# Kernel tuning notes

Measured on AMD Instinct MI355X. Metric: run time of the kernel, lower is better.

Reference implementation:

```python
import jax, jax.numpy as jnp
import numpy as np

EPS_BN = 1e-5
NEG = -9e15


def _bn_train(x, g, b):
    # x: [B, C, N]; training-mode BatchNorm1d with batch stats (biased var)
    m = jnp.mean(x, axis=(0, 2), keepdims=True)
    v = jnp.mean((x - m) ** 2, axis=(0, 2), keepdims=True)
    return (x - m) * jax.lax.rsqrt(v + EPS_BN) * g[None, :, None] + b[None, :, None]


def _conv1x1(w, x, b=None):
    # w: [O, C], x: [B, C, N] -> [B, O, N]
    y = jnp.einsum('oc,bcn->bon', w, x)
    if b is not None:
        y = y + b[None, :, None]
    return y


def _sa_layer(x, maskb, qk_w, v_w, v_b, t_w, t_b, bn_g, bn_b):
    # x: [B, C, N], maskb: [B, N] bool
    q = jnp.einsum('hc,bcn->bhn', qk_w, x)          # shared q/k weights
    energy = jnp.einsum('bhn,bhm->bnm', q, q)        # [B, N, N]
    pair = maskb[:, :, None] & maskb[:, None, :]
    energy = jnp.where(pair, energy, NEG)
    attn = jax.nn.softmax(energy, axis=-1)
    attn = attn / (1e-9 + jnp.sum(attn, axis=1, keepdims=True))  # L1 renorm over dim=1
    x_v = _conv1x1(v_w, x, v_b)                      # [B, C, N]
    x_r = jnp.einsum('bcn,bnm->bcm', x_v, attn)      # bmm(x_v, attention)
    t = _conv1x1(t_w, x - x_r, t_b)
    x_r = jax.nn.relu(_bn_train(t, bn_g, bn_b))
    return x + x_r


def setup_inputs() -> dict:
    key = jax.random.key(0)
    ks = jax.random.split(key, 16)
    B, C, N = 16, 256, 2048
    H = C // 4
    s = 0.05
    inp = {
        'x': jax.random.normal(ks[0], (B, C, N), jnp.float32),
        'mask': jax.random.randint(ks[1], (B, N), 0, 2, jnp.int32),
        'conv1_w': jax.random.normal(ks[2], (C, C), jnp.float32) * s,
        'conv2_w': jax.random.normal(ks[3], (C, C), jnp.float32) * s,
        'bn1_g': jnp.ones((C,), jnp.float32),
        'bn1_b': jnp.zeros((C,), jnp.float32),
        'bn2_g': jnp.ones((C,), jnp.float32),
        'bn2_b': jnp.zeros((C,), jnp.float32),
        'sa_qk_w': jax.random.normal(ks[4], (4, H, C), jnp.float32) * s,
        'sa_v_w': jax.random.normal(ks[5], (4, C, C), jnp.float32) * s,
        'sa_v_b': jax.random.normal(ks[6], (4, C), jnp.float32) * s,
        'sa_t_w': jax.random.normal(ks[7], (4, C, C), jnp.float32) * s,
        'sa_t_b': jax.random.normal(ks[8], (4, C), jnp.float32) * s,
        'sa_bn_g': jnp.ones((4, C), jnp.float32),
        'sa_bn_b': jnp.zeros((4, C), jnp.float32),
    }
    return inp


def reference(x, mask, conv1_w, conv2_w, bn1_g, bn1_b, bn2_g, bn2_b,
              sa_qk_w, sa_v_w, sa_v_b, sa_t_w, sa_t_b, sa_bn_g, sa_bn_b):
    maskb = mask.astype(bool)
    x = jax.nn.relu(_bn_train(_conv1x1(conv1_w, x), bn1_g, bn1_b))
    x = jax.nn.relu(_bn_train(_conv1x1(conv2_w, x), bn2_g, bn2_b))
    outs = []
    for i in range(4):
        x = _sa_layer(x, maskb, sa_qk_w[i], sa_v_w[i], sa_v_b[i],
                      sa_t_w[i], sa_t_b[i], sa_bn_g[i], sa_bn_b[i])
        outs.append(x)
    return jnp.concatenate(outs, axis=1)  # [B, 4C, N]
```

## Files before the change

kernel.cpp:

```cpp
#include <hip/hip_runtime.h>
#include <math.h>

#define BB 16
#define CC 256
#define NN 2048
#define HH 64
#define NEGV (-9.0e15f)
#define ATTSC 4096.0f
#define ATTINV (1.0f/4096.0f)

typedef _Float16 f16x8 __attribute__((ext_vector_type(8)));
typedef float f32x4 __attribute__((ext_vector_type(4)));

__device__ __forceinline__ f32x4 mfma16(f16x8 a, f16x8 b, f32x4 c) {
  return __builtin_amdgcn_mfma_f32_16x16x32_f16(a, b, c, 0, 0, 0);
}
__device__ __forceinline__ unsigned short f2h(float f) {
  _Float16 h = (_Float16)f;
  return __builtin_bit_cast(unsigned short, h);
}
__device__ __forceinline__ float h2f(unsigned short u) {
  return (float)__builtin_bit_cast(_Float16, u);
}
__device__ __forceinline__ unsigned short* sp(unsigned short* base, int row, int colh) {
  return (unsigned short*)((char*)base + (row << 7) + (((colh << 1)) ^ ((row & 7) << 4)));
}
__device__ __forceinline__ const unsigned short* spc(const unsigned short* base, int row, int colh) {
  return (const unsigned short*)((const char*)base + (row << 7) + (((colh << 1)) ^ ((row & 7) << 4)));
}

__global__ __launch_bounds__(256)
void castw_kernel(const float* __restrict__ in, unsigned short* __restrict__ out, int n)
{
  const int i = blockIdx.x*256 + threadIdx.x;
  if (i < n) out[i] = f2h(in[i]);
}

__global__ __launch_bounds__(256)
void tcast_kernel(const float* __restrict__ src, long sstride,
                  unsigned short* __restrict__ dst)
{
  const int b = blockIdx.z, n0 = blockIdx.x*64, c0 = blockIdx.y*64;
  const int t = threadIdx.x;
  __shared__ float tile[64][66];
  const float* sb = src + (long)b*sstride;
  #pragma unroll
  for (int p = 0; p < 4; p++) {
    const int cr = (t>>4) + p*16;
    const int nq = (t&15)*4;
    const float4 v = *(const float4*)&sb[(long)(c0+cr)*NN + n0 + nq];
    tile[cr][nq+0] = v.x; tile[cr][nq+1] = v.y;
    tile[cr][nq+2] = v.z; tile[cr][nq+3] = v.w;
  }
  __syncthreads();
  unsigned short* db = dst + (long)b*NN*CC;
  #pragma unroll
  for (int p = 0; p < 4; p++) {
    const int nr = (t>>4) + p*16;
    const int cq = (t&15)*4;
    ushort4 o;
    o.x = f2h(tile[cq+0][nr]); o.y = f2h(tile[cq+1][nr]);
    o.z = f2h(tile[cq+2][nr]); o.w = f2h(tile[cq+3][nr]);
    *(ushort4*)&db[(long)(n0+nr)*CC + c0 + cq] = o;
  }
}

__global__ __launch_bounds__(256)
void gemm_xw_kernel(const unsigned short* __restrict__ A,
                    const unsigned short* __restrict__ W,
                    const float* __restrict__ bias,
                    unsigned short* __restrict__ out, int ocols)
{
  const int n0 = blockIdx.x*64, o0 = blockIdx.y*64, b = blockIdx.z;
  const int t = threadIdx.x;
  const int w = t >> 6, l = t & 63, lr = l & 15, lg = l >> 4;
  const int wr = w >> 1, wc = w & 1;
  __shared__ unsigned short Al[64][72];
  __shared__ unsigned short Bl[64][72];
  const unsigned short* Ab = A + ((long)b*NN + n0)*CC;
  const int srow = t >> 3, sg = t & 7;
  f32x4 acc[2][2];
  #pragma unroll
  for (int i = 0; i < 2; i++)
    #pragma unroll
    for (int j = 0; j < 2; j++) acc[i][j] = f32x4{0.f,0.f,0.f,0.f};

  for (int kt = 0; kt < 4; kt++) {
    const int k0 = kt*64;
    const uint4 a0 = *(const uint4*)&Ab[(long)srow*CC + k0 + sg*8];
    const uint4 a1 = *(const uint4*)&Ab[(long)(srow+32)*CC + k0 + sg*8];
    const uint4 w0 = *(const uint4*)&W[(long)(o0+srow)*CC + k0 + sg*8];
    const uint4 w1 = *(const uint4*)&W[(long)(o0+srow+32)*CC + k0 + sg*8];
    __syncthreads();
    *(uint4*)&Al[srow][sg*8] = a0;  *(uint4*)&Al[srow+32][sg*8] = a1;
    *(uint4*)&Bl[srow][sg*8] = w0;  *(uint4*)&Bl[srow+32][sg*8] = w1;
    __syncthreads();
    #pragma unroll
    for (int kf = 0; kf < 2; kf++) {
      f16x8 af0 = *(const f16x8*)&Al[wr*32 + lr]     [kf*32 + lg*8];
      f16x8 af1 = *(const f16x8*)&Al[wr*32 + 16 + lr][kf*32 + lg*8];
      f16x8 bf0 = *(const f16x8*)&Bl[wc*32 + lr]     [kf*32 + lg*8];
      f16x8 bf1 = *(const f16x8*)&Bl[wc*32 + 16 + lr][kf*32 + lg*8];
      acc[0][0] = mfma16(af0, bf0, acc[0][0]);
      acc[0][1] = mfma16(af0, bf1, acc[0][1]);
      acc[1][0] = mfma16(af1, bf0, acc[1][0]);
      acc[1][1] = mfma16(af1, bf1, acc[1][1]);
    }
  }
  #pragma unroll
  for (int j = 0; j < 2; j++) {
    const int oc = o0 + wc*32 + j*16 + lr;
    const float bo = bias ? bias[oc] : 0.f;
    #pragma unroll
    for (int i = 0; i < 2; i++) {
      const int nb = n0 + wr*32 + i*16 + lg*4;
      #pragma unroll
      for (int r = 0; r < 4; r++)
        out[((long)b*NN + nb + r)*ocols + oc] = f2h(acc[i][j][r] + bo);
    }
  }
}

__global__ __launch_bounds__(256)
void gemm_wx_kernel(const unsigned short* __restrict__ W,
                    const unsigned short* __restrict__ X,
                    const float* __restrict__ bias,
                    unsigned short* __restrict__ out)
{
  const int n0 = blockIdx.x*64, o0 = blockIdx.y*64, b = blockIdx.z;
  const int t = threadIdx.x;
  const int w = t >> 6, l = t & 63, lr = l & 15, lg = l >> 4;
  const int wr = w >> 1, wc = w & 1;
  __shared__ unsigned short Al[64][72];
  __shared__ unsigned short Bl[64][72];
  const unsigned short* Xb = X + ((long)b*NN + n0)*CC;
  const int srow = t >> 3, sg = t & 7;
  f32x4 acc[2][2];
  #pragma unroll
  for (int i = 0; i < 2; i++)
    #pragma unroll
    for (int j = 0; j < 2; j++) acc[i][j] = f32x4{0.f,0.f,0.f,0.f};

  for (int kt = 0; kt < 4; kt++) {
    const int k0 = kt*64;
    const uint4 w0 = *(const uint4*)&W[(long)(o0+srow)*CC + k0 + sg*8];
    const uint4 w1 = *(const uint4*)&W[(long)(o0+srow+32)*CC + k0 + sg*8];
    const uint4 x0 = *(const uint4*)&Xb[(long)srow*CC + k0 + sg*8];
    const uint4 x1 = *(const uint4*)&Xb[(long)(srow+32)*CC + k0 + sg*8];
    __syncthreads();
    *(uint4*)&Al[srow][sg*8] = w0;  *(uint4*)&Al[srow+32][sg*8] = w1;
    *(uint4*)&Bl[srow][sg*8] = x0;  *(uint4*)&Bl[srow+32][sg*8] = x1;
    __syncthreads();
    #pragma unroll
    for (int kf = 0; kf < 2; kf++) {
      f16x8 af0 = *(const f16x8*)&Al[wr*32 + lr]     [kf*32 + lg*8];
      f16x8 af1 = *(const f16x8*)&Al[wr*32 + 16 + lr][kf*32 + lg*8];
      f16x8 bf0 = *(const f16x8*)&Bl[wc*32 + lr]     [kf*32 + lg*8];
      f16x8 bf1 = *(const f16x8*)&Bl[wc*32 + 16 + lr][kf*32 + lg*8];
      acc[0][0] = mfma16(af0, bf0, acc[0][0]);
      acc[0][1] = mfma16(af0, bf1, acc[0][1]);
      acc[1][0] = mfma16(af1, bf0, acc[1][0]);
      acc[1][1] = mfma16(af1, bf1, acc[1][1]);
    }
  }
  #pragma unroll
  for (int j = 0; j < 2; j++) {
    const int nc = n0 + wc*32 + j*16 + lr;
    #pragma unroll
    for (int i = 0; i < 2; i++) {
      #pragma unroll
      for (int r = 0; r < 4; r++) {
        const int oc = o0 + wr*32 + i*16 + lg*4 + r;
        out[((long)b*CC + oc)*NN + nc] = f2h(acc[i][j][r] + bias[oc]);
      }
    }
  }
}

__global__ __launch_bounds__(256)
void rowstat_kernel(const unsigned short* __restrict__ qT, const int* __restrict__ mask,
                    float* __restrict__ rmax, float* __restrict__ rinv)
{
  const int bid = blockIdx.x;
  const int swz = (bid & 7)*64 + (bid >> 3);
  const int b  = swz >> 5;
  const int n0 = (swz & 31) * 64;
  const int t = threadIdx.x, w = t>>6, l = t&63, lr = l&15, lg = l>>4;
  __shared__ unsigned short qs[64*64];
  __shared__ int ml[64];
  const int srow = t>>3, sg = t&7;
  const unsigned short* qbase = qT + (long)b*NN*HH;
  *(uint4*)sp(qs, srow,    sg*8) = *(const uint4*)&qbase[(long)(n0+srow)*HH + sg*8];
  *(uint4*)sp(qs, srow+32, sg*8) = *(const uint4*)&qbase[(long)(n0+srow+32)*HH + sg*8];
  int maskn[4];
  #pragma unroll
  for (int r = 0; r < 4; r++) maskn[r] = mask[(long)b*NN + n0 + w*16 + lg*4 + r];
  __syncthreads();
  f16x8 af0 = *(const f16x8*)spc(qs, w*16 + lr, lg*8);
  f16x8 af1 = *(const f16x8*)spc(qs, w*16 + lr, 32 + lg*8);
  float mx[4], sm[4];
  #pragma unroll
  for (int r = 0; r < 4; r++) { mx[r] = -INFINITY; sm[r] = 0.f; }

  for (int m0 = 0; m0 < NN; m0 += 64) {
    __syncthreads();
    *(uint4*)sp(qs, srow,    sg*8) = *(const uint4*)&qbase[(long)(m0+srow)*HH + sg*8];
    *(uint4*)sp(qs, srow+32, sg*8) = *(const uint4*)&qbase[(long)(m0+srow+32)*HH + sg*8];
    if (t < 64) ml[t] = mask[(long)b*NN + m0 + t];
    __syncthreads();
    float sv[4][4];
    #pragma unroll
    for (int tm = 0; tm < 4; tm++) {
      f32x4 s = f32x4{0.f,0.f,0.f,0.f};
      s = mfma16(af0, *(const f16x8*)spc(qs, tm*16 + lr, lg*8),      s);
      s = mfma16(af1, *(const f16x8*)spc(qs, tm*16 + lr, 32 + lg*8), s);
      const int cm = ml[tm*16 + lr];
      #pragma unroll
      for (int r = 0; r < 4; r++) sv[tm][r] = (maskn[r] && cm) ? s[r] : NEGV;
    }
    #pragma unroll
    for (int r = 0; r < 4; r++) {
      const float tmx = fmaxf(fmaxf(sv[0][r], sv[1][r]), fmaxf(sv[2][r], sv[3][r]));
      const float nm  = fmaxf(mx[r], tmx);
      sm[r] = sm[r]*__expf(mx[r]-nm)
            + __expf(sv[0][r]-nm) + __expf(sv[1][r]-nm)
            + __expf(sv[2][r]-nm) + __expf(sv[3][r]-nm);
      mx[r] = nm;
    }
  }
  #pragma unroll
  for (int off = 1; off < 16; off <<= 1) {
    #pragma unroll
    for (int r = 0; r < 4; r++) {
      const float om = __shfl_xor(mx[r], off, 64);
      const float os = __shfl_xor(sm[r], off, 64);
      const float nm = fmaxf(mx[r], om);
      sm[r] = sm[r]*__expf(mx[r]-nm) + os*__expf(om-nm);
      mx[r] = nm;
    }
  }
  if (lr == 0) {
    #pragma unroll
    for (int r = 0; r < 4; r++) {
      const long idx = (long)b*NN + n0 + w*16 + lg*4 + r;
      rmax[idx] = mx[r];
      rinv[idx] = 1.f/sm[r];
    }
  }
}

__global__ __launch_bounds__(256)
void yatt_kernel(const unsigned short* __restrict__ qT, const unsigned short* __restrict__ xv,
                 const int* __restrict__ mask, const float* __restrict__ rmax,
                 const float* __restrict__ rinv, unsigned short* __restrict__ xrTh,
                 float* __restrict__ csum)
{
  const int bid = blockIdx.x;
  const int swz = (bid & 7)*64 + (bid >> 3);
  const int b  = swz >> 5;
  const int m0 = (swz & 31) * 64;
  const int t = threadIdx.x, w = t>>6, l = t&63, lr = l&15, lg = l>>4;
  __shared__ unsigned short qn[64*64];
  __shared__ unsigned short at[64*64];
  __shared__ float rml[64], ril[64];
  __shared__ int mrl[64];
  const int srow = t>>3, sg = t&7;
  const unsigned short* qbase = qT + (long)b*NN*HH;
  const unsigned short* xvb = xv + (long)b*CC*NN;

  *(uint4*)sp(at, srow,    sg*8) = *(const uint4*)&qbase[(long)(m0+srow)*HH + sg*8];
  *(uint4*)sp(at, srow+32, sg*8) = *(const uint4*)&qbase[(long)(m0+srow+32)*HH + sg*8];
  int maskm[4];
  #pragma unroll
  for (int r = 0; r < 4; r++) maskm[r] = mask[(long)b*NN + m0 + w*16 + lg*4 + r];
  __syncthreads();
  f16x8 am0 = *(const f16x8*)spc(at, w*16 + lr, lg*8);
  f16x8 am1 = *(const f16x8*)spc(at, w*16 + lr, 32 + lg*8);

  f32x4 acc[4][4];
  #pragma unroll
  for (int mi = 0; mi < 4; mi++)
    #pragma unroll
    for (int ci = 0; ci < 4; ci++) acc[mi][ci] = f32x4{0.f,0.f,0.f,0.f};
  float cs[4] = {0.f, 0.f, 0.f, 0.f};

  for (int nc = 0; nc < NN; nc += 64) {
    __syncthreads();
    *(uint4*)sp(qn, srow,    sg*8) = *(const uint4*)&qbase[(long)(nc+srow)*HH + sg*8];
    *(uint4*)sp(qn, srow+32, sg*8) = *(const uint4*)&qbase[(long)(nc+srow+32)*HH + sg*8];
    if (t < 64) {
      rml[t] = rmax[(long)b*NN + nc + t];
      ril[t] = rinv[(long)b*NN + nc + t];
      mrl[t] = mask[(long)b*NN + nc + t];
    }
    f16x8 xb0[4], xb1[4];
    #pragma unroll
    for (int ci = 0; ci < 4; ci++) {
      const unsigned short* xp = &xvb[(long)(w*64 + ci*16 + lr)*NN + nc];
      xb0[ci] = *(const f16x8*)(xp + lg*8);
      xb1[ci] = *(const f16x8*)(xp + 32 + lg*8);
    }
    __syncthreads();
    #pragma unroll
    for (int tn = 0; tn < 4; tn++) {
      f32x4 s = f32x4{0.f,0.f,0.f,0.f};
      s = mfma16(am0, *(const f16x8*)spc(qn, tn*16 + lr, lg*8),      s);
      s = mfma16(am1, *(const f16x8*)spc(qn, tn*16 + lr, 32 + lg*8), s);
      const int nn = tn*16 + lr;
      const int cm = mrl[nn];
      const float rm = rml[nn], ri = ril[nn];
      #pragma unroll
      for (int r = 0; r < 4; r++) {
        const float vm = (maskm[r] && cm) ? s[r] : NEGV;
        const float a_ = __expf(vm - rm) * ri;
        cs[r] += a_;
        *sp(at, w*16 + lg*4 + r, nn) = f2h(a_ * ATTSC);
      }
    }
    __syncthreads();
    {
      f16x8 aa[4];
      #pragma unroll
      for (int mi = 0; mi < 4; mi++) aa[mi] = *(const f16x8*)spc(at, mi*16 + lr, lg*8);
      #pragma unroll
      for (int ci = 0; ci < 4; ci++)
        #pragma unroll
        for (int mi = 0; mi < 4; mi++)
          acc[mi][ci] = mfma16(aa[mi], xb0[ci], acc[mi][ci]);
      #pragma unroll
      for (int mi = 0; mi < 4; mi++) aa[mi] = *(const f16x8*)spc(at, mi*16 + lr, 32 + lg*8);
      #pragma unroll
      for (int ci = 0; ci < 4; ci++)
        #pragma unroll
        for (int mi = 0; mi < 4; mi++)
          acc[mi][ci] = mfma16(aa[mi], xb1[ci], acc[mi][ci]);
    }
  }
  #pragma unroll
  for (int mi = 0; mi < 4; mi++)
    #pragma unroll
    for (int ci = 0; ci < 4; ci++)
      #pragma unroll
      for (int r = 0; r < 4; r++)
        xrTh[((long)b*NN + m0 + mi*16 + lg*4 + r)*CC + w*64 + ci*16 + lr] =
            f2h(acc[mi][ci][r] * ATTINV);
  #pragma unroll
  for (int off = 1; off < 16; off <<= 1) {
    #pragma unroll
    for (int r = 0; r < 4; r++) cs[r] += __shfl_xor(cs[r], off, 64);
  }
  if (lr == 0) {
    #pragma unroll
    for (int r = 0; r < 4; r++)
      csum[(long)b*NN + m0 + w*16 + lg*4 + r] = cs[r];
  }
}

__global__ __launch_bounds__(256)
void diff_kernel(const unsigned short* __restrict__ xT, const unsigned short* __restrict__ xrTh,
                 const float* __restrict__ csumv, unsigned short* __restrict__ dT)
{
  const long i = (long)blockIdx.x*256 + threadIdx.x;
  const long base = i*8;
  const long row = base >> 8;
  const float inv = 1.f/(1e-9f + csumv[row]);
  const uint4 xu = *(const uint4*)&xT[base];
  const uint4 yu = *(const uint4*)&xrTh[base];
  const unsigned short* xs = (const unsigned short*)&xu;
  const unsigned short* ys = (const unsigned short*)&yu;
  uint4 ou;
  unsigned short* os = (unsigned short*)&ou;
  #pragma unroll
  for (int j = 0; j < 8; j++) os[j] = f2h(h2f(xs[j]) - h2f(ys[j])*inv);
  *(uint4*)&dT[base] = ou;
}

__global__ __launch_bounds__(256)
void bnstatsA_kernel(const unsigned short* __restrict__ tTh, float* __restrict__ part)
{
  const int k = blockIdx.x;
  const int c = threadIdx.x;
  float s = 0.f, sq = 0.f;
  const long r0 = (long)k*128;
  for (int r = 0; r < 128; r++) {
    const float v = h2f(tTh[(r0 + r)*CC + c]);
    s += v; sq += v*v;
  }
  part[(long)k*CC + c] = s;
  part[(long)(256 + k)*CC + c] = sq;
}

__global__ __launch_bounds__(1024)
void bnstatsB_kernel(const float* __restrict__ part,
                     float* __restrict__ mean, float* __restrict__ istd)
{
  const int t = threadIdx.x, c = t & 255, q = t >> 8;
  float s = 0.f, sq = 0.f;
  for (int k = q*64; k < q*64 + 64; k++) {
    s  += part[(long)k*CC + c];
    sq += part[(long)(256 + k)*CC + c];
  }
  __shared__ float ls[4][256], lq[4][256];
  ls[q][c] = s; lq[q][c] = sq;
  __syncthreads();
  if (q == 0) {
    s  = ls[0][c] + ls[1][c] + ls[2][c] + ls[3][c];
    sq = lq[0][c] + lq[1][c] + lq[2][c] + lq[3][c];
    const float mu = s / (float)(BB*NN);
    mean[c] = mu;
    istd[c] = rsqrtf(sq/(float)(BB*NN) - mu*mu + 1e-5f);
  }
}

__global__ __launch_bounds__(256)
void bnapplyA_kernel(const unsigned short* __restrict__ tTh, const float* __restrict__ mean,
                     const float* __restrict__ istd, const float* __restrict__ g,
                     const float* __restrict__ bt, unsigned short* __restrict__ xTo)
{
  __shared__ float sc[CC], sh[CC];
  const int t = threadIdx.x;
  {
    const float is = istd[t], gg = g[t];
    sc[t] = is*gg; sh[t] = bt[t] - mean[t]*is*gg;
  }
  __syncthreads();
  const long i = (long)blockIdx.x*256 + t;
  const long base = i*8;
  const int c8 = (int)(base & 255);
  const uint4 v = *(const uint4*)&tTh[base];
  const unsigned short* hs = (const unsigned short*)&v;
  uint4 ou;
  unsigned short* os = (unsigned short*)&ou;
  #pragma unroll
  for (int j = 0; j < 8; j++)
    os[j] = f2h(fmaxf(h2f(hs[j])*sc[c8+j] + sh[c8+j], 0.f));
  *(uint4*)&xTo[base] = ou;
}

__global__ __launch_bounds__(256)
void bnfuse_kernel(const unsigned short* __restrict__ tTh, const float* __restrict__ mean,
                   const float* __restrict__ istd, const float* __restrict__ g,
                   const float* __restrict__ bt, const float* __restrict__ resid,
                   long rstride, float* __restrict__ outp, long ostride,
                   unsigned short* __restrict__ xtn)
{
  const int b = blockIdx.z, n0 = blockIdx.x*64, c0 = blockIdx.y*64;
  const int t = threadIdx.x;
  __shared__ float tile[64][66];
  const unsigned short* tb_ = tTh + ((long)b*NN + n0)*CC;
  const int cq = (t&15)*4;
  float scv[4], shv[4];
  #pragma unroll
  for (int j = 0; j < 4; j++) {
    const int c = c0 + cq + j;
    const float is = istd[c], gg = g[c];
    scv[j] = is*gg; shv[j] = bt[c] - mean[c]*is*gg;
  }
  #pragma unroll
  for (int p = 0; p < 4; p++) {
    const int nr = (t>>4) + p*16;
    const ushort4 v = *(const ushort4*)&tb_[(long)nr*CC + c0 + cq];
    tile[cq+0][nr] = fmaxf(h2f(v.x)*scv[0] + shv[0], 0.f);
    tile[cq+1][nr] = fmaxf(h2f(v.y)*scv[1] + shv[1], 0.f);
    tile[cq+2][nr] = fmaxf(h2f(v.z)*scv[2] + shv[2], 0.f);
    tile[cq+3][nr] = fmaxf(h2f(v.w)*scv[3] + shv[3], 0.f);
  }
  __syncthreads();
  const int nq = (t&15)*4;
  #pragma unroll
  for (int p = 0; p < 4; p++) {
    const int cr = (t>>4) + p*16;
    float4 o;
    o.x = tile[cr][nq+0]; o.y = tile[cr][nq+1];
    o.z = tile[cr][nq+2]; o.w = tile[cr][nq+3];
    if (resid) {
      const float4 rv = *(const float4*)&resid[(long)b*rstride + (long)(c0+cr)*NN + n0 + nq];
      o.x += rv.x; o.y += rv.y; o.z += rv.z; o.w += rv.w;
    }
    *(float4*)&outp[(long)b*ostride + (long)(c0+cr)*NN + n0 + nq] = o;
    tile[cr][nq+0] = o.x; tile[cr][nq+1] = o.y;
    tile[cr][nq+2] = o.z; tile[cr][nq+3] = o.w;
  }
  if (xtn) {
    __syncthreads();
    #pragma unroll
    for (int p = 0; p < 4; p++) {
      const int nr = (t>>4) + p*16;
      ushort4 o;
      o.x = f2h(tile[cq+0][nr]); o.y = f2h(tile[cq+1][nr]);
      o.z = f2h(tile[cq+2][nr]); o.w = f2h(tile[cq+3][nr]);
      *(ushort4*)&xtn[((long)b*NN + n0+nr)*CC + c0 + cq] = o;
    }
  }
}

extern "C" void kernel_launch(void* const* d_in, const int* in_sizes, int n_in,
                              void* d_out, int out_size, void* d_ws, size_t ws_size,
                              hipStream_t stream)
{
  const float* x_in   = (const float*)d_in[0];
  const int*   mask   = (const int*)d_in[1];
  const float* conv1w = (const float*)d_in[2];
  const float* conv2w = (const float*)d_in[3];
  const float* bn1g   = (const float*)d_in[4];
  const float* bn1b   = (const float*)d_in[5];
  const float* bn2g   = (const float*)d_in[6];
  const float* bn2b   = (const float*)d_in[7];
  const float* qkw    = (const float*)d_in[8];
  const float* vw     = (const float*)d_in[9];
  const float* vb     = (const float*)d_in[10];
  const float* tw     = (const float*)d_in[11];
  const float* tb     = (const float*)d_in[12];
  const float* bng    = (const float*)d_in[13];
  const float* bnb    = (const float*)d_in[14];
  float* out = (float*)d_out;

  const long BCN = (long)BB*CC*NN;
  const long CN  = (long)CC*NN;
  char* p = (char*)d_ws;
  unsigned short* xTa  = (unsigned short*)p; p += BCN*2;
  unsigned short* xTb  = (unsigned short*)p; p += BCN*2;
  unsigned short* qTb  = (unsigned short*)p; p += (long)BB*NN*HH*2;
  unsigned short* xvb  = (unsigned short*)p; p += BCN*2;
  unsigned short* tTh  = (unsigned short*)p; p += BCN*2;
  unsigned short* xrTh = (unsigned short*)p; p += BCN*2;
  float* xbuf  = (float*)p; p += BCN*4;
  float* rmaxb = (float*)p; p += (long)BB*NN*4;
  float* rinvb = (float*)p; p += (long)BB*NN*4;
  float* csumb = (float*)p; p += (long)BB*NN*4;
  float* partb = (float*)p; p += 512L*CC*4;
  float* meanb = (float*)p; p += CC*4;
  float* istdb = (float*)p; p += CC*4;
  unsigned short* wc1 = (unsigned short*)p; p += (long)CC*CC*2;
  unsigned short* wc2 = (unsigned short*)p; p += (long)CC*CC*2;
  unsigned short* wqk = (unsigned short*)p; p += 4L*HH*CC*2;
  unsigned short* wv  = (unsigned short*)p; p += 4L*CC*CC*2;
  unsigned short* wt  = (unsigned short*)p; p += 4L*CC*CC*2;

  const dim3 gT(NN/64, CC/64, BB);
  const dim3 gQ(NN/64, 1, BB);
  const dim3 gAtt(512);
  const dim3 blk(256);

  castw_kernel<<<dim3(256), blk, 0, stream>>>(conv1w, wc1, CC*CC);
  castw_kernel<<<dim3(256), blk, 0, stream>>>(conv2w, wc2, CC*CC);
  castw_kernel<<<dim3(256), blk, 0, stream>>>(qkw, wqk, 4*HH*CC);
  castw_kernel<<<dim3(1024), blk, 0, stream>>>(vw, wv, 4*CC*CC);
  castw_kernel<<<dim3(1024), blk, 0, stream>>>(tw, wt, 4*CC*CC);

  tcast_kernel<<<gT, blk, 0, stream>>>(x_in, CN, xTa);
  gemm_xw_kernel<<<gT, blk, 0, stream>>>(xTa, wc1, nullptr, tTh, CC);
  bnstatsA_kernel<<<dim3(256), blk, 0, stream>>>(tTh, partb);
  bnstatsB_kernel<<<dim3(1), dim3(1024), 0, stream>>>(partb, meanb, istdb);
  bnapplyA_kernel<<<dim3(4096), blk, 0, stream>>>(tTh, meanb, istdb, bn1g, bn1b, xTb);
  gemm_xw_kernel<<<gT, blk, 0, stream>>>(xTb, wc2, nullptr, tTh, CC);
  bnstatsA_kernel<<<dim3(256), blk, 0, stream>>>(tTh, partb);
  bnstatsB_kernel<<<dim3(1), dim3(1024), 0, stream>>>(partb, meanb, istdb);
  bnfuse_kernel<<<gT, blk, 0, stream>>>(tTh, meanb, istdb, bn2g, bn2b,
                                        nullptr, 0, xbuf, CN, xTa);

  unsigned short* cur = xTa;
  unsigned short* nxt = xTb;
  for (int i = 0; i < 4; i++) {
    gemm_xw_kernel<<<gQ, blk, 0, stream>>>(cur, wqk + (long)i*HH*CC, nullptr, qTb, HH);
    rowstat_kernel<<<gAtt, blk, 0, stream>>>(qTb, mask, rmaxb, rinvb);
    gemm_wx_kernel<<<gT, blk, 0, stream>>>(wv + (long)i*CC*CC, cur, vb + (long)i*CC, xvb);
    yatt_kernel<<<gAtt, blk, 0, stream>>>(qTb, xvb, mask, rmaxb, rinvb, xrTh, csumb);
    diff_kernel<<<dim3(4096), blk, 0, stream>>>(cur, xrTh, csumb, xvb);
    gemm_xw_kernel<<<gT, blk, 0, stream>>>(xvb, wt + (long)i*CC*CC, tb + (long)i*CC, tTh, CC);
    bnstatsA_kernel<<<dim3(256), blk, 0, stream>>>(tTh, partb);
    bnstatsB_kernel<<<dim3(1), dim3(1024), 0, stream>>>(partb, meanb, istdb);
    const float* resid = (i == 0) ? xbuf : (out + (long)(i-1)*CN);
    const long rstr = (i == 0) ? CN : 4*CN;
    bnfuse_kernel<<<gT, blk, 0, stream>>>(tTh, meanb, istdb,
                                          bng + (long)i*CC, bnb + (long)i*CC,
                                          resid, rstr, out + (long)i*CN, 4*CN,
                                          (i < 3) ? nxt : nullptr);
    unsigned short* tmp = cur; cur = nxt; nxt = tmp;
  }

  (void)in_sizes; (void)n_in; (void)out_size; (void)ws_size;
}
```

Measured before the change: 773.3 us.

## Split attention rowstat and yatt across more blocks, fuse diff into T-conv GEMM

The rowstat kernel now splits the key dimension into four partial passes (2048 blocks). It reads q straight from global memory instead of LDS, and a new rowcomb kernel merges the partial max/sum pairs. The yatt kernel splits the channel dimension into two halves (1024 blocks) and computes keys from register-resident m-side q. Its column-sum reduction now goes through LDS. The separate diff kernel is removed by folding the x - xr/csum subtraction into a new gemm_dxw GEMM's operand load, in exchange for recomputing QK^T twice in yatt and an extra launch.

New measurement: 1.131 ms. 1.46x slower.

```diff
diff --git a/kernel.cpp b/kernel.cpp
--- a/kernel.cpp
+++ b/kernel.cpp
@@ -122,6 +122,82 @@
 }
 
 __global__ __launch_bounds__(256)
+void gemm_dxw_kernel(const unsigned short* __restrict__ X,
+                     const unsigned short* __restrict__ XR,
+                     const float* __restrict__ csumv,
+                     const unsigned short* __restrict__ W,
+                     const float* __restrict__ bias,
+                     unsigned short* __restrict__ out)
+{
+  const int n0 = blockIdx.x*64, o0 = blockIdx.y*64, b = blockIdx.z;
+  const int t = threadIdx.x;
+  const int w = t >> 6, l = t & 63, lr = l & 15, lg = l >> 4;
+  const int wr = w >> 1, wc = w & 1;
+  __shared__ unsigned short Al[64][72];
+  __shared__ unsigned short Bl[64][72];
+  const unsigned short* Xb  = X  + ((long)b*NN + n0)*CC;
+  const unsigned short* XRb = XR + ((long)b*NN + n0)*CC;
+  const int srow = t >> 3, sg = t & 7;
+  const float inv0 = 1.f/(1e-9f + csumv[(long)b*NN + n0 + srow]);
+  const float inv1 = 1.f/(1e-9f + csumv[(long)b*NN + n0 + srow + 32]);
+  f32x4 acc[2][2];
+  #pragma unroll
+  for (int i = 0; i < 2; i++)
+    #pragma unroll
+    for (int j = 0; j < 2; j++) acc[i][j] = f32x4{0.f,0.f,0.f,0.f};
+
+  for (int kt = 0; kt < 4; kt++) {
+    const int k0 = kt*64;
+    const uint4 xa  = *(const uint4*)&Xb [(long)srow*CC + k0 + sg*8];
+    const uint4 xra = *(const uint4*)&XRb[(long)srow*CC + k0 + sg*8];
+    const uint4 xb_ = *(const uint4*)&Xb [(long)(srow+32)*CC + k0 + sg*8];
+    const uint4 xrb = *(const uint4*)&XRb[(long)(srow+32)*CC + k0 + sg*8];
+    const uint4 w0 = *(const uint4*)&W[(long)(o0+srow)*CC + k0 + sg*8];
+    const uint4 w1 = *(const uint4*)&W[(long)(o0+srow+32)*CC + k0 + sg*8];
+    uint4 da, db_;
+    {
+      const unsigned short* xs = (const unsigned short*)&xa;
+      const unsigned short* rs = (const unsigned short*)&xra;
+      unsigned short* ds = (unsigned short*)&da;
+      #pragma unroll
+      for (int j = 0; j < 8; j++) ds[j] = f2h(h2f(xs[j]) - h2f(rs[j])*inv0);
+      xs = (const unsigned short*)&xb_;
+      rs = (const unsigned short*)&xrb;
+      ds = (unsigned short*)&db_;
+      #pragma unroll
+      for (int j = 0; j < 8; j++) ds[j] = f2h(h2f(xs[j]) - h2f(rs[j])*inv1);
+    }
+    __syncthreads();
+    *(uint4*)&Al[srow][sg*8] = da;  *(uint4*)&Al[srow+32][sg*8] = db_;
+    *(uint4*)&Bl[srow][sg*8] = w0;  *(uint4*)&Bl[srow+32][sg*8] = w1;
+    __syncthreads();
+    #pragma unroll
+    for (int kf = 0; kf < 2; kf++) {
+      f16x8 af0 = *(const f16x8*)&Al[wr*32 + lr]     [kf*32 + lg*8];
+      f16x8 af1 = *(const f16x8*)&Al[wr*32 + 16 + lr][kf*32 + lg*8];
+      f16x8 bf0 = *(const f16x8*)&Bl[wc*32 + lr]     [kf*32 + lg*8];
+      f16x8 bf1 = *(const f16x8*)&Bl[wc*32 + 16 + lr][kf*32 + lg*8];
+      acc[0][0] = mfma16(af0, bf0, acc[0][0]);
+      acc[0][1] = mfma16(af0, bf1, acc[0][1]);
+      acc[1][0] = mfma16(af1, bf0, acc[1][0]);
+      acc[1][1] = mfma16(af1, bf1, acc[1][1]);
+    }
+  }
+  #pragma unroll
+  for (int j = 0; j < 2; j++) {
+    const int oc = o0 + wc*32 + j*16 + lr;
+    const float bo = bias[oc];
+    #pragma unroll
+    for (int i = 0; i < 2; i++) {
+      const int nb = n0 + wr*32 + i*16 + lg*4;
+      #pragma unroll
+      for (int r = 0; r < 4; r++)
+        out[((long)b*NN + nb + r)*CC + oc] = f2h(acc[i][j][r] + bo);
+    }
+  }
+}
+
+__global__ __launch_bounds__(256)
 void gemm_wx_kernel(const unsigned short* __restrict__ W,
                     const unsigned short* __restrict__ X,
                     const float* __restrict__ bias,
@@ -179,44 +255,39 @@
 
 __global__ __launch_bounds__(256)
 void rowstat_kernel(const unsigned short* __restrict__ qT, const int* __restrict__ mask,
-                    float* __restrict__ rmax, float* __restrict__ rinv)
+                    float* __restrict__ pmax, float* __restrict__ psum)
 {
   const int bid = blockIdx.x;
-  const int swz = (bid & 7)*64 + (bid >> 3);
-  const int b  = swz >> 5;
-  const int n0 = (swz & 31) * 64;
+  const int sbid = (bid & 7)*256 + (bid >> 3);
+  const int b = sbid >> 7;
+  const int r_ = sbid & 127;
+  const int split = r_ >> 5;
+  const int nt4 = r_ & 31;
   const int t = threadIdx.x, w = t>>6, l = t&63, lr = l&15, lg = l>>4;
-  __shared__ unsigned short qs[64*64];
-  __shared__ int ml[64];
-  const int srow = t>>3, sg = t&7;
+  const int n0w = nt4*64 + w*16;
   const unsigned short* qbase = qT + (long)b*NN*HH;
-  *(uint4*)sp(qs, srow,    sg*8) = *(const uint4*)&qbase[(long)(n0+srow)*HH + sg*8];
-  *(uint4*)sp(qs, srow+32, sg*8) = *(const uint4*)&qbase[(long)(n0+srow+32)*HH + sg*8];
-  int maskn[4];
-  #pragma unroll
-  for (int r = 0; r < 4; r++) maskn[r] = mask[(long)b*NN + n0 + w*16 + lg*4 + r];
-  __syncthreads();
-  f16x8 af0 = *(const f16x8*)spc(qs, w*16 + lr, lg*8);
-  f16x8 af1 = *(const f16x8*)spc(qs, w*16 + lr, 32 + lg*8);
+  const unsigned short* qnp = &qbase[(long)(n0w + lr)*HH];
+  const f16x8 a0 = *(const f16x8*)(qnp + lg*8);
+  const f16x8 a1 = *(const f16x8*)(qnp + 32 + lg*8);
+  const int4 mn4 = *(const int4*)&mask[(long)b*NN + n0w + lg*4];
+  const int mn[4] = {mn4.x, mn4.y, mn4.z, mn4.w};
   float mx[4], sm[4];
   #pragma unroll
   for (int r = 0; r < 4; r++) { mx[r] = -INFINITY; sm[r] = 0.f; }
 
-  for (int m0 = 0; m0 < NN; m0 += 64) {
-    __syncthreads();
-    *(uint4*)sp(qs, srow,    sg*8) = *(const uint4*)&qbase[(long)(m0+srow)*HH + sg*8];
-    *(uint4*)sp(qs, srow+32, sg*8) = *(const uint4*)&qbase[(long)(m0+srow+32)*HH + sg*8];
-    if (t < 64) ml[t] = mask[(long)b*NN + m0 + t];
-    __syncthreads();
+  for (int c = 0; c < 8; c++) {
+    const int m0 = split*512 + c*64;
     float sv[4][4];
     #pragma unroll
     for (int tm = 0; tm < 4; tm++) {
-      f32x4 s = f32x4{0.f,0.f,0.f,0.f};
-      s = mfma16(af0, *(const f16x8*)spc(qs, tm*16 + lr, lg*8),      s);
-      s = mfma16(af1, *(const f16x8*)spc(qs, tm*16 + lr, 32 + lg*8), s);
-      const int cm = ml[tm*16 + lr];
-      #pragma unroll
-      for (int r = 0; r < 4; r++) sv[tm][r] = (maskn[r] && cm) ? s[r] : NEGV;
+      const unsigned short* qmp = &qbase[(long)(m0 + tm*16 + lr)*HH];
+      f16x8 b0 = *(const f16x8*)(qmp + lg*8);
+      f16x8 b1 = *(const f16x8*)(qmp + 32 + lg*8);
+      f32x4 s = mfma16(a0, b0, f32x4{0.f,0.f,0.f,0.f});
+      s = mfma16(a1, b1, s);
+      const int cm = mask[(long)b*NN + m0 + tm*16 + lr];
+      #pragma unroll
+      for (int r = 0; r < 4; r++) sv[tm][r] = (mn[r] && cm) ? s[r] : NEGV;
     }
     #pragma unroll
     for (int r = 0; r < 4; r++) {
@@ -242,11 +313,27 @@
   if (lr == 0) {
     #pragma unroll
     for (int r = 0; r < 4; r++) {
-      const long idx = (long)b*NN + n0 + w*16 + lg*4 + r;
-      rmax[idx] = mx[r];
-      rinv[idx] = 1.f/sm[r];
-    }
-  }
+      const long idx = (long)split*BB*NN + (long)b*NN + n0w + lg*4 + r;
+      pmax[idx] = mx[r];
+      psum[idx] = sm[r];
+    }
+  }
+}
+
+__global__ __launch_bounds__(256)
+void rowcomb_kernel(const float* __restrict__ pmax, const float* __restrict__ psum,
+                    float* __restrict__ rmaxo, float* __restrict__ rinvo)
+{
+  const long i = (long)blockIdx.x*256 + threadIdx.x;
+  const long BN = (long)BB*NN;
+  float m = pmax[i];
+  #pragma unroll
+  for (int k = 1; k < 4; k++) m = fmaxf(m, pmax[(long)k*BN + i]);
+  float s = 0.f;
+  #pragma unroll
+  for (int k = 0; k < 4; k++) s += psum[(long)k*BN + i]*__expf(pmax[(long)k*BN + i] - m);
+  rmaxo[i] = m;
+  rinvo[i] = 1.f/s;
 }
 
 __global__ __launch_bounds__(256)
@@ -256,123 +343,109 @@
                  float* __restrict__ csum)
 {
   const int bid = blockIdx.x;
-  const int swz = (bid & 7)*64 + (bid >> 3);
-  const int b  = swz >> 5;
-  const int m0 = (swz & 31) * 64;
+  const int swz = (bid & 7)*128 + (bid >> 3);
+  const int b  = swz >> 6;
+  const int r_ = swz & 63;
+  const int m0 = (r_ >> 1) * 64;
+  const int ch = r_ & 1;
   const int t = threadIdx.x, w = t>>6, l = t&63, lr = l&15, lg = l>>4;
-  __shared__ unsigned short qn[64*64];
+
   __shared__ unsigned short at[64*64];
-  __shared__ float rml[64], ril[64];
-  __shared__ int mrl[64];
-  const int srow = t>>3, sg = t&7;
+  __shared__ float csred[4][4][16];
+
   const unsigned short* qbase = qT + (long)b*NN*HH;
   const unsigned short* xvb = xv + (long)b*CC*NN;
 
-  *(uint4*)sp(at, srow,    sg*8) = *(const uint4*)&qbase[(long)(m0+srow)*HH + sg*8];
-  *(uint4*)sp(at, srow+32, sg*8) = *(const uint4*)&qbase[(long)(m0+srow+32)*HH + sg*8];
-  int maskm[4];
-  #pragma unroll
-  for (int r = 0; r < 4; r++) maskm[r] = mask[(long)b*NN + m0 + w*16 + lg*4 + r];
-  __syncthreads();
-  f16x8 am0 = *(const f16x8*)spc(at, w*16 + lr, lg*8);
-  f16x8 am1 = *(const f16x8*)spc(at, w*16 + lr, 32 + lg*8);
-
-  f32x4 acc[4][4];
+  f16x8 bq0[4], bq1[4];
+  int mcolv[4];
+  #pragma unroll
+  for (int tm = 0; tm < 4; tm++) {
+    const unsigned short* qp = &qbase[(long)(m0 + tm*16 + lr)*HH];
+    bq0[tm] = *(const f16x8*)(qp + lg*8);
+    bq1[tm] = *(const f16x8*)(qp + 32 + lg*8);
+    mcolv[tm] = mask[(long)b*NN + m0 + tm*16 + lr];
+  }
+
+  f32x4 acc[4][2];
   #pragma unroll
   for (int mi = 0; mi < 4; mi++)
     #pragma unroll
-    for (int ci = 0; ci < 4; ci++) acc[mi][ci] = f32x4{0.f,0.f,0.f,0.f};
+    for (int ci = 0; ci < 2; ci++) acc[mi][ci] = f32x4{0.f,0.f,0.f,0.f};
   float cs[4] = {0.f, 0.f, 0.f, 0.f};
+  const int nb = w*16 + lg*4;
 
   for (int nc = 0; nc < NN; nc += 64) {
-    __syncthreads();
-    *(uint4*)sp(qn, srow,    sg*8) = *(const uint4*)&qbase[(long)(nc+srow)*HH + sg*8];
-    *(uint4*)sp(qn, srow+32, sg*8) = *(const uint4*)&qbase[(long)(nc+srow+32)*HH + sg*8];
-    if (t < 64) {
-      rml[t] = rmax[(long)b*NN + nc + t];
-      ril[t] = rinv[(long)b*NN + nc + t];
-      mrl[t] = mask[(long)b*NN + nc + t];
-    }
-    f16x8 xb0[4], xb1[4];
-    #pragma unroll
-    for (int ci = 0; ci < 4; ci++) {
-      const unsigned short* xp = &xvb[(long)(w*64 + ci*16 + lr)*NN + nc];
+    const unsigned short* qnp = &qbase[(long)(nc + w*16 + lr)*HH];
+    const f16x8 a0 = *(const f16x8*)(qnp + lg*8);
+    const f16x8 a1 = *(const f16x8*)(qnp + 32 + lg*8);
+    f16x8 xb0[2], xb1[2];
+    #pragma unroll
+    for (int ci = 0; ci < 2; ci++) {
+      const unsigned short* xp = &xvb[(long)(ch*128 + w*32 + ci*16 + lr)*NN + nc];
       xb0[ci] = *(const f16x8*)(xp + lg*8);
       xb1[ci] = *(const f16x8*)(xp + 32 + lg*8);
     }
-    __syncthreads();
-    #pragma unroll
-    for (int tn = 0; tn < 4; tn++) {
-      f32x4 s = f32x4{0.f,0.f,0.f,0.f};
-      s = mfma16(am0, *(const f16x8*)spc(qn, tn*16 + lr, lg*8),      s);
-      s = mfma16(am1, *(const f16x8*)spc(qn, tn*16 + lr, 32 + lg*8), s);
-      const int nn = tn*16 + lr;
-      const int cm = mrl[nn];
-      const float rm = rml[nn], ri = ril[nn];
+    const float4 rm4 = *(const float4*)&rmax[(long)b*NN + nc + nb];
+    const float4 ri4 = *(const float4*)&rinv[(long)b*NN + nc + nb];
+    const int4   mn4 = *(const int4*)&mask[(long)b*NN + nc + nb];
+    const float rmv[4] = {rm4.x, rm4.y, rm4.z, rm4.w};
+    const float riv[4] = {ri4.x, ri4.y, ri4.z, ri4.w};
+    const int   mnv[4] = {mn4.x, mn4.y, mn4.z, mn4.w};
+
+    ushort4 pk[4];
+    #pragma unroll
+    for (int tm = 0; tm < 4; tm++) {
+      f32x4 s = mfma16(a0, bq0[tm], f32x4{0.f,0.f,0.f,0.f});
+      s = mfma16(a1, bq1[tm], s);
+      unsigned short* po = (unsigned short*)&pk[tm];
       #pragma unroll
       for (int r = 0; r < 4; r++) {
-        const float vm = (maskm[r] && cm) ? s[r] : NEGV;
-        const float a_ = __expf(vm - rm) * ri;
-        cs[r] += a_;
-        *sp(at, w*16 + lg*4 + r, nn) = f2h(a_ * ATTSC);
+        const float vm = (mnv[r] && mcolv[tm]) ? s[r] : NEGV;
+        const float a_ = __expf(vm - rmv[r]) * riv[r];
+        cs[tm] += a_;
+        po[r] = f2h(a_ * ATTSC);
       }
     }
     __syncthreads();
-    {
-      f16x8 aa[4];
-      #pragma unroll
-      for (int mi = 0; mi < 4; mi++) aa[mi] = *(const f16x8*)spc(at, mi*16 + lr, lg*8);
-      #pragma unroll
-      for (int ci = 0; ci < 4; ci++)
-        #pragma unroll
-        for (int mi = 0; mi < 4; mi++)
-          acc[mi][ci] = mfma16(aa[mi], xb0[ci], acc[mi][ci]);
-      #pragma unroll
-      for (int mi = 0; mi < 4; mi++) aa[mi] = *(const f16x8*)spc(at, mi*16 + lr, 32 + lg*8);
-      #pragma unroll
-      for (int ci = 0; ci < 4; ci++)
-        #pragma unroll
-        for (int mi = 0; mi < 4; mi++)
-          acc[mi][ci] = mfma16(aa[mi], xb1[ci], acc[mi][ci]);
-    }
-  }
+    #pragma unroll
+    for (int tm = 0; tm < 4; tm++)
+      *(ushort4*)sp(at, tm*16 + lr, nb) = pk[tm];
+    __syncthreads();
+    #pragma unroll
+    for (int mi = 0; mi < 4; mi++) {
+      const f16x8 aa0 = *(const f16x8*)spc(at, mi*16 + lr, lg*8);
+      const f16x8 aa1 = *(const f16x8*)spc(at, mi*16 + lr, 32 + lg*8);
+      acc[mi][0] = mfma16(aa0, xb0[0], acc[mi][0]);
+      acc[mi][1] = mfma16(aa0, xb0[1], acc[mi][1]);
+      acc[mi][0] = mfma16(aa1, xb1[0], acc[mi][0]);
+      acc[mi][1] = mfma16(aa1, xb1[1], acc[mi][1]);
+    }
+  }
+
   #pragma unroll
   for (int mi = 0; mi < 4; mi++)
     #pragma unroll
-    for (int ci = 0; ci < 4; ci++)
+    for (int ci = 0; ci < 2; ci++)
       #pragma unroll
       for (int r = 0; r < 4; r++)
-        xrTh[((long)b*NN + m0 + mi*16 + lg*4 + r)*CC + w*64 + ci*16 + lr] =
+        xrTh[((long)b*NN + m0 + mi*16 + lg*4 + r)*CC + ch*128 + w*32 + ci*16 + lr] =
             f2h(acc[mi][ci][r] * ATTINV);
-  #pragma unroll
-  for (int off = 1; off < 16; off <<= 1) {
-    #pragma unroll
-    for (int r = 0; r < 4; r++) cs[r] += __shfl_xor(cs[r], off, 64);
-  }
-  if (lr == 0) {
-    #pragma unroll
-    for (int r = 0; r < 4; r++)
-      csum[(long)b*NN + m0 + w*16 + lg*4 + r] = cs[r];
-  }
-}
-
-__global__ __launch_bounds__(256)
-void diff_kernel(const unsigned short* __restrict__ xT, const unsigned short* __restrict__ xrTh,
-                 const float* __restrict__ csumv, unsigned short* __restrict__ dT)
-{
-  const long i = (long)blockIdx.x*256 + threadIdx.x;
-  const long base = i*8;
-  const long row = base >> 8;
-  const float inv = 1.f/(1e-9f + csumv[row]);
-  const uint4 xu = *(const uint4*)&xT[base];
-  const uint4 yu = *(const uint4*)&xrTh[base];
-  const unsigned short* xs = (const unsigned short*)&xu;
-  const unsigned short* ys = (const unsigned short*)&yu;
-  uint4 ou;
-  unsigned short* os = (unsigned short*)&ou;
-  #pragma unroll
-  for (int j = 0; j < 8; j++) os[j] = f2h(h2f(xs[j]) - h2f(ys[j])*inv);
-  *(uint4*)&dT[base] = ou;
+
+  if (ch == 0) {
+    #pragma unroll
+    for (int tm = 0; tm < 4; tm++) {
+      cs[tm] += __shfl_xor(cs[tm], 16, 64);
+      cs[tm] += __shfl_xor(cs[tm], 32, 64);
+      if (lg == 0) csred[tm][w][lr] = cs[tm];
+    }
+    __syncthreads();
+    if (t < 64) {
+      const int tm = t >> 4, mr = t & 15;
+      const float v = csred[tm][0][mr] + csred[tm][1][mr]
+                    + csred[tm][2][mr] + csred[tm][3][mr];
+      csum[(long)b*NN + m0 + tm*16 + mr] = v;
+    }
+  }
 }
 
 __global__ __launch_bounds__(256)
@@ -517,6 +590,7 @@
 
   const long BCN = (long)BB*CC*NN;
   const long CN  = (long)CC*NN;
+  const long BN  = (long)BB*NN;
   char* p = (char*)d_ws;
   unsigned short* xTa  = (unsigned short*)p; p += BCN*2;
   unsigned short* xTb  = (unsigned short*)p; p += BCN*2;
@@ -525,9 +599,11 @@
   unsigned short* tTh  = (unsigned short*)p; p += BCN*2;
   unsigned short* xrTh = (unsigned short*)p; p += BCN*2;
   float* xbuf  = (float*)p; p += BCN*4;
-  float* rmaxb = (float*)p; p += (long)BB*NN*4;
-  float* rinvb = (float*)p; p += (long)BB*NN*4;
-  float* csumb = (float*)p; p += (long)BB*NN*4;
+  float* rmaxb = (float*)p; p += BN*4;
+  float* rinvb = (float*)p; p += BN*4;
+  float* csumb = (float*)p; p += BN*4;
+  float* pmaxb = (float*)p; p += 4*BN*4;
+  float* psumb = (float*)p; p += 4*BN*4;
   float* partb = (float*)p; p += 512L*CC*4;
   float* meanb = (float*)p; p += CC*4;
   float* istdb = (float*)p; p += CC*4;
@@ -539,7 +615,6 @@
 
   const dim3 gT(NN/64, CC/64, BB);
   const dim3 gQ(NN/64, 1, BB);
-  const dim3 gAtt(512);
   const dim3 blk(256);
 
   castw_kernel<<<dim3(256), blk, 0, stream>>>(conv1w, wc1, CC*CC);
@@ -563,11 +638,12 @@
   unsigned short* nxt = xTb;
   for (int i = 0; i < 4; i++) {
     gemm_xw_kernel<<<gQ, blk, 0, stream>>>(cur, wqk + (long)i*HH*CC, nullptr, qTb, HH);
-    rowstat_kernel<<<gAtt, blk, 0, stream>>>(qTb, mask, rmaxb, rinvb);
+    rowstat_kernel<<<dim3(2048), blk, 0, stream>>>(qTb, mask, pmaxb, psumb);
     gemm_wx_kernel<<<gT, blk, 0, stream>>>(wv + (long)i*CC*CC, cur, vb + (long)i*CC, xvb);
-    yatt_kernel<<<gAtt, blk, 0, stream>>>(qTb, xvb, mask, rmaxb, rinvb, xrTh, csumb);
-    diff_kernel<<<dim3(4096), blk, 0, stream>>>(cur, xrTh, csumb, xvb);
-    gemm_xw_kernel<<<gT, blk, 0, stream>>>(xvb, wt + (long)i*CC*CC, tb + (long)i*CC, tTh, CC);
+    rowcomb_kernel<<<dim3(128), blk, 0, stream>>>(pmaxb, psumb, rmaxb, rinvb);
+    yatt_kernel<<<dim3(1024), blk, 0, stream>>>(qTb, xvb, mask, rmaxb, rinvb, xrTh, csumb);
+    gemm_dxw_kernel<<<gT, blk, 0, stream>>>(cur, xrTh, csumb,
+                                            wt + (long)i*CC*CC, tb + (long)i*CC, tTh);
     bnstatsA_kernel<<<dim3(256), blk, 0, stream>>>(tTh, partb);
     bnstatsB_kernel<<<dim3(1), dim3(1024), 0, stream>>>(partb, meanb, istdb);
     const float* resid = (i == 0) ? xbuf : (out + (long)(i-1)*CN);
```
